# Optimization experiments

Hardware: AMD Instinct MI355X
Metric: run time of the kernel (lower is better)

Reference implementation:

```python
import jax, jax.numpy as jnp
import numpy as np
from jax.scipy.special import betainc, ndtri, ndtr

DF = 4.0        # fixed_df
ALPHA = 0.94    # ewma_alpha
EPS = 1e-5      # scale_eps
UCLIP = 1e-6    # cdf clamp


def _ewma_loc_scale(x_hist):
    # x_hist: [B, T, D]
    loc = jnp.mean(x_hist, axis=1, keepdims=True)            # [B,1,D]
    c2 = jnp.square(x_hist - loc)                            # [B,T,D]
    c2_t = jnp.swapaxes(c2, 0, 1)                            # [T,B,D] for scan over time

    def step(var, c):
        var = ALPHA * var + (1.0 - ALPHA) * c
        return var, var

    _, tail = jax.lax.scan(step, c2_t[0], c2_t[1:])
    ewma = jnp.concatenate([c2_t[:1], tail], axis=0)         # [T,B,D]
    ewma = jnp.swapaxes(ewma, 0, 1)                          # [B,T,D]
    scale_hist = jnp.maximum(jnp.sqrt(ewma * (DF - 2.0) / DF), EPS)
    return loc, scale_hist


def _student_t_cdf(x, loc, scale):
    # Student-t CDF via regularized incomplete beta: df fixed scalar constant
    t = (x - loc) / scale
    w = DF / (DF + t * t)
    p = 0.5 * betainc(DF / 2.0, 0.5, w)
    u = jnp.where(t <= 0.0, p, 1.0 - p)
    return jnp.clip(u, UCLIP, 1.0 - UCLIP)


def _student_t_ppf_df4(u):
    # Exact closed form for df=4 (Shaw): a = 4u(1-u),
    # q = sign(u-1/2) * 2*sqrt(cos(arccos(sqrt(a))/3)/sqrt(a) - 1)
    a = jnp.clip(4.0 * u * (1.0 - u), UCLIP, 1.0)
    sa = jnp.sqrt(a)
    inner = jnp.cos(jnp.arccos(sa) / 3.0) / sa - 1.0
    q = 2.0 * jnp.sqrt(jnp.maximum(inner, 0.0))
    return jnp.sign(u - 0.5) * q


def setup_inputs() -> dict:
    key = jax.random.key(0)
    k1, k2 = jax.random.split(key)
    B, T, P, D = 128, 2048, 64, 128
    x_hist = jax.random.normal(k1, (B, T, D), dtype=jnp.float32)
    z_future = jax.random.normal(k2, (B, P, D), dtype=jnp.float32)
    return {"x_hist": x_hist, "z_future": z_future}


def reference(x_hist, z_future):
    # _fit_student_t: loc + EWMA variance -> per-step scale
    loc, scale_hist = _ewma_loc_scale(x_hist)                # [B,1,D], [B,T,D]
    scale_future = scale_hist[:, -1:, :]                     # [B,1,D]
    # _to_gaussian(x_hist): t CDF -> standard normal ICDF
    x_hist_norm = ndtri(_student_t_cdf(x_hist, loc, scale_hist))  # [B,T,D]
    # _from_gaussian(z_future): normal CDF -> t PPF (df=4 closed form)
    u = jnp.clip(ndtr(z_future), UCLIP, 1.0 - UCLIP)
    forecasts = _student_t_ppf_df4(u) * scale_future + loc   # [B,P,D]
    # concat along time for a single output tensor [B, T+P, D]
    return jnp.concatenate([x_hist_norm, forecasts], axis=1)
```

## Files before the change

### kernel.cpp

```cpp
#include <hip/hip_runtime.h>
#include <math.h>

namespace {
constexpr int B = 128;
constexpr int T = 2048;
constexpr int D = 128;
constexpr int P = 64;
constexpr int TOUT = T + P;
constexpr int NC = 32;
constexpr int L = T / NC;
constexpr float ALPHA = 0.94f;
constexpr float OMA = (float)(1.0 - 0.94);
constexpr float OMA_HALF = 0.03f;
constexpr float UCLIP = 1e-6f;
constexpr float INV_SQRT2 = 0.70710678118654752f;
}

__device__ __forceinline__ float t_to_z_direct(float y, float vv) {
    float it = __builtin_amdgcn_rsqf(vv);
    float t  = y * it;
    float q  = t * t;
    float rc = __builtin_amdgcn_rcpf(8.0f + q);
    float p;
    p = fmaf(-1453.744128f, rc, 610.201088f);
    p = fmaf(p, rc, -98.038976f);
    p = fmaf(p, rc, 10.835976f);
    p = fmaf(p, rc, 0.280213f);
    return t * p;
}

__global__ __launch_bounds__(128) void kA(const float* __restrict__ x,
                                          float* __restrict__ Spart,
                                          float* __restrict__ l1e,
                                          float* __restrict__ l2e) {
    const int c = blockIdx.x;
    const int b = blockIdx.y;
    const int d = threadIdx.x;

    const float* xp = x + ((size_t)b * T + (size_t)c * L) * D + d;

    float x0 = xp[0];
    float sum = x0;
    float l1, l2;
    if (c == 0) { l1 = x0;        l2 = x0 * x0; }
    else        { l1 = OMA * x0;  l2 = OMA * (x0 * x0); }

    for (int k = 1; k < L; ++k) {
        float xv = xp[(size_t)k * D];
        sum += xv;
        l1 = fmaf(ALPHA, l1, OMA * xv);
        l2 = fmaf(ALPHA, l2, OMA * (xv * xv));
    }

    const size_t o = ((size_t)b * NC + c) * D + d;
    Spart[o] = sum;
    l1e[o]   = l1;
    l2e[o]   = l2;
}

__global__ __launch_bounds__(256) void kB(const float* Spart,
                                          const float* l1e,
                                          const float* l2e,
                                          float* carry1,
                                          float* carry2,
                                          float* __restrict__ loc,
                                          float* __restrict__ scf) {
    const int tid = blockIdx.x * blockDim.x + threadIdx.x;
    if (tid >= B * D) return;
    const int b = tid / D;
    const int d = tid % D;

    const float alphaL = (float)pow((double)ALPHA, (double)L);

    float sum = 0.0f, e1 = 0.0f, e2 = 0.0f;
    for (int c = 0; c < NC; ++c) {
        const size_t o = ((size_t)b * NC + c) * D + d;
        float sp = Spart[o];
        float t1 = l1e[o];
        float t2 = l2e[o];
        carry1[o] = e1;
        carry2[o] = e2;
        sum += sp;
        e1 = t1 + alphaL * e1;
        e2 = t2 + alphaL * e2;
    }

    const float mu = sum * (1.0f / (float)T);
    loc[tid] = mu;
    float ew = fmaxf(fmaf(mu, mu, fmaf(-2.0f * mu, e1, e2)), 0.0f);
    scf[tid] = fmaxf(sqrtf(0.5f * ew), 1e-5f);

    for (int c = 0; c < NC; ++c) {
        const size_t o = ((size_t)b * NC + c) * D + d;
        float c1 = carry1[o];
        float c2 = carry2[o];
        carry1[o] = fmaf(-mu, c1, 0.5f * c2);
    }
}

__global__ __launch_bounds__(128) void kC(const float* __restrict__ x,
                                          const float* __restrict__ crwb,
                                          const float* __restrict__ locg,
                                          float* __restrict__ out) {
    const int c = blockIdx.x;
    const int b = blockIdx.y;
    const int d = threadIdx.x;

    const size_t co = ((size_t)b * NC + c) * D + d;
    const float crw   = crwb[co];
    const float mu    = locg[b * D + d];
    const float twomu = 2.0f * mu;
    const float mu2h  = 0.5f * mu * mu;

    const float* xp = x   + ((size_t)b * T    + (size_t)c * L) * D + d;
    float*       op = out + ((size_t)b * TOUT + (size_t)c * L) * D + d;

    float xv = xp[0];
    float g  = xv * (xv - twomu);
    float base = (c == 0) ? 0.5f * g : OMA_HALF * g;
    float s  = fmaf(ALPHA, crw, base);
    float vv = fmaxf(s + mu2h, 1e-10f);
    __builtin_nontemporal_store(t_to_z_direct(xv - mu, vv), &op[0]);

    for (int k = 1; k < L; ++k) {
        xv = xp[(size_t)k * D];
        g  = xv * (xv - twomu);
        s  = fmaf(ALPHA, s, OMA_HALF * g);
        vv = fmaxf(s + mu2h, 1e-10f);
        __builtin_nontemporal_store(t_to_z_direct(xv - mu, vv), &op[(size_t)k * D]);
    }
}

__global__ __launch_bounds__(256) void kD(const float* __restrict__ zf,
                                          const float* __restrict__ loc,
                                          const float* __restrict__ scf,
                                          float* __restrict__ out) {
    const int idx = blockIdx.x * blockDim.x + threadIdx.x;
    if (idx >= B * P * D) return;
    const int d  = idx % D;
    const int bp = idx / D;
    const int p  = bp % P;
    const int b  = bp / P;

    float zv = zf[idx];
    float u = 0.5f * erfcf(-zv * INV_SQRT2);
    u = fminf(fmaxf(u, UCLIP), 1.0f - UCLIP);

    float a = 4.0f * u * (1.0f - u);
    a = fminf(fmaxf(a, UCLIP), 1.0f);
    float sa = sqrtf(a);
    float inner = cosf(acosf(sa) * (1.0f / 3.0f)) / sa - 1.0f;
    float qv = 2.0f * sqrtf(fmaxf(inner, 0.0f));

    float sgn = (u > 0.5f) ? 1.0f : ((u < 0.5f) ? -1.0f : 0.0f);
    float val = sgn * qv * scf[b * D + d] + loc[b * D + d];

    __builtin_nontemporal_store(val, &out[((size_t)b * TOUT + T + p) * D + d]);
}

extern "C" void kernel_launch(void* const* d_in, const int* in_sizes, int n_in,
                              void* d_out, int out_size, void* d_ws, size_t ws_size,
                              hipStream_t stream) {
    const float* x  = (const float*)d_in[0];
    const float* zf = (const float*)d_in[1];
    float* out = (float*)d_out;

    float* ws = (float*)d_ws;
    const size_t NCH = (size_t)B * NC * D;
    float* Spart  = ws;
    float* l1e    = Spart + NCH;
    float* l2e    = l1e + NCH;
    float* loc    = l2e + NCH;
    float* scf    = loc + (size_t)B * D;
    float* carry1 = Spart;
    float* carry2 = l1e;

    kA<<<dim3(NC, B), 128, 0, stream>>>(x, Spart, l1e, l2e);
    kB<<<(B * D + 255) / 256, 256, 0, stream>>>(Spart, l1e, l2e, carry1, carry2, loc, scf);
    kC<<<dim3(NC, B), 128, 0, stream>>>(x, carry1, loc, out);
    kD<<<(B * P * D + 255) / 256, 256, 0, stream>>>(zf, loc, scf, out);
}
```

Before: 83.33 us.

## Fold carry scan and forecast kernel into the main transform kernel

Removes the separate carry-scan kernel (kB) and forecast kernel (kD). Each kC block now redundantly scans all chunk partials for its batch to derive the mean and its own carry. The last chunk block also computes the forecast rows. This cuts two launches and the workspace round trips. In exchange, every block re-reads NC×3 partials, and the last-chunk blocks take on serialized forecast work, which adds tail imbalance.

```diff
diff --git a/kernel.cpp b/kernel.cpp
--- a/kernel.cpp
+++ b/kernel.cpp
@@ -58,57 +58,30 @@
     l2e[o]   = l2;
 }
 
-__global__ __launch_bounds__(256) void kB(const float* Spart,
-                                          const float* l1e,
-                                          const float* l2e,
-                                          float* carry1,
-                                          float* carry2,
-                                          float* __restrict__ loc,
-                                          float* __restrict__ scf) {
-    const int tid = blockIdx.x * blockDim.x + threadIdx.x;
-    if (tid >= B * D) return;
-    const int b = tid / D;
-    const int d = tid % D;
-
-    const float alphaL = (float)pow((double)ALPHA, (double)L);
-
-    float sum = 0.0f, e1 = 0.0f, e2 = 0.0f;
-    for (int c = 0; c < NC; ++c) {
-        const size_t o = ((size_t)b * NC + c) * D + d;
-        float sp = Spart[o];
-        float t1 = l1e[o];
-        float t2 = l2e[o];
-        carry1[o] = e1;
-        carry2[o] = e2;
-        sum += sp;
-        e1 = t1 + alphaL * e1;
-        e2 = t2 + alphaL * e2;
-    }
-
-    const float mu = sum * (1.0f / (float)T);
-    loc[tid] = mu;
-    float ew = fmaxf(fmaf(mu, mu, fmaf(-2.0f * mu, e1, e2)), 0.0f);
-    scf[tid] = fmaxf(sqrtf(0.5f * ew), 1e-5f);
-
-    for (int c = 0; c < NC; ++c) {
-        const size_t o = ((size_t)b * NC + c) * D + d;
-        float c1 = carry1[o];
-        float c2 = carry2[o];
-        carry1[o] = fmaf(-mu, c1, 0.5f * c2);
-    }
-}
-
 __global__ __launch_bounds__(128) void kC(const float* __restrict__ x,
-                                          const float* __restrict__ crwb,
-                                          const float* __restrict__ locg,
+                                          const float* __restrict__ Spart,
+                                          const float* __restrict__ l1e,
+                                          const float* __restrict__ l2e,
+                                          const float* __restrict__ zf,
                                           float* __restrict__ out) {
     const int c = blockIdx.x;
     const int b = blockIdx.y;
     const int d = threadIdx.x;
 
-    const size_t co = ((size_t)b * NC + c) * D + d;
-    const float crw   = crwb[co];
-    const float mu    = locg[b * D + d];
+    const float alphaL = (float)pow((double)ALPHA, (double)L);
+
+    float sum = 0.0f, e1 = 0.0f, e2 = 0.0f;
+    float cr1 = 0.0f, cr2 = 0.0f;
+    for (int j = 0; j < NC; ++j) {
+        const size_t o = ((size_t)b * NC + j) * D + d;
+        sum += Spart[o];
+        if (j == c) { cr1 = e1; cr2 = e2; }
+        e1 = l1e[o] + alphaL * e1;
+        e2 = l2e[o] + alphaL * e2;
+    }
+    const float mu = sum * (1.0f / (float)T);
+    const float crw = fmaf(-mu, cr1, 0.5f * cr2);
+
     const float twomu = 2.0f * mu;
     const float mu2h  = 0.5f * mu * mu;
 
@@ -129,33 +102,31 @@
         vv = fmaxf(s + mu2h, 1e-10f);
         __builtin_nontemporal_store(t_to_z_direct(xv - mu, vv), &op[(size_t)k * D]);
     }
-}
 
-__global__ __launch_bounds__(256) void kD(const float* __restrict__ zf,
-                                          const float* __restrict__ loc,
-                                          const float* __restrict__ scf,
-                                          float* __restrict__ out) {
-    const int idx = blockIdx.x * blockDim.x + threadIdx.x;
-    if (idx >= B * P * D) return;
-    const int d  = idx % D;
-    const int bp = idx / D;
-    const int p  = bp % P;
-    const int b  = bp / P;
+    if (c == NC - 1) {
+        float ew = fmaxf(fmaf(mu, mu, fmaf(-2.0f * mu, e1, e2)), 0.0f);
+        float scf = fmaxf(sqrtf(0.5f * ew), 1e-5f);
 
-    float zv = zf[idx];
-    float u = 0.5f * erfcf(-zv * INV_SQRT2);
-    u = fminf(fmaxf(u, UCLIP), 1.0f - UCLIP);
+        const float* zp = zf  + (size_t)b * P * D + d;
+        float*       fp = out + ((size_t)b * TOUT + T) * D + d;
 
-    float a = 4.0f * u * (1.0f - u);
-    a = fminf(fmaxf(a, UCLIP), 1.0f);
-    float sa = sqrtf(a);
-    float inner = cosf(acosf(sa) * (1.0f / 3.0f)) / sa - 1.0f;
-    float qv = 2.0f * sqrtf(fmaxf(inner, 0.0f));
+        for (int p = 0; p < P; ++p) {
+            float zv = zp[(size_t)p * D];
+            float u = 0.5f * erfcf(-zv * INV_SQRT2);
+            u = fminf(fmaxf(u, UCLIP), 1.0f - UCLIP);
 
-    float sgn = (u > 0.5f) ? 1.0f : ((u < 0.5f) ? -1.0f : 0.0f);
-    float val = sgn * qv * scf[b * D + d] + loc[b * D + d];
+            float a = 4.0f * u * (1.0f - u);
+            a = fminf(fmaxf(a, UCLIP), 1.0f);
+            float sa = sqrtf(a);
+            float inner = cosf(acosf(sa) * (1.0f / 3.0f)) / sa - 1.0f;
+            float qv = 2.0f * sqrtf(fmaxf(inner, 0.0f));
 
-    __builtin_nontemporal_store(val, &out[((size_t)b * TOUT + T + p) * D + d]);
+            float sgn = (u > 0.5f) ? 1.0f : ((u < 0.5f) ? -1.0f : 0.0f);
+            float val = fmaf(sgn * qv, scf, mu);
+
+            __builtin_nontemporal_store(val, &fp[(size_t)p * D]);
+        }
+    }
 }
 
 extern "C" void kernel_launch(void* const* d_in, const int* in_sizes, int n_in,
@@ -167,16 +138,10 @@
 
     float* ws = (float*)d_ws;
     const size_t NCH = (size_t)B * NC * D;
-    float* Spart  = ws;
-    float* l1e    = Spart + NCH;
-    float* l2e    = l1e + NCH;
-    float* loc    = l2e + NCH;
-    float* scf    = loc + (size_t)B * D;
-    float* carry1 = Spart;
-    float* carry2 = l1e;
+    float* Spart = ws;
+    float* l1e   = Spart + NCH;
+    float* l2e   = l1e + NCH;
 
     kA<<<dim3(NC, B), 128, 0, stream>>>(x, Spart, l1e, l2e);
-    kB<<<(B * D + 255) / 256, 256, 0, stream>>>(Spart, l1e, l2e, carry1, carry2, loc, scf);
-    kC<<<dim3(NC, B), 128, 0, stream>>>(x, carry1, loc, out);
-    kD<<<(B * P * D + 255) / 256, 256, 0, stream>>>(zf, loc, scf, out);
+    kC<<<dim3(NC, B), 128, 0, stream>>>(x, Spart, l1e, l2e, zf, out);
 }
```

Result: slower. 176.4 us (+111.7%).
